# Performance work log

Hardware: AMD Instinct MI355X
Metric: run time of the kernel (lower is better)

Reference implementation:

```python
import jax, jax.numpy as jnp
import numpy as np

B, L = 4, 2048
D_MODEL, D_STATE, D_CONV, EXPAND = 1024, 16, 4, 2
D_INNER = EXPAND * D_MODEL
DT_RANK = D_MODEL // 16  # mamba-ssm default dt_rank = ceil(d_model/16)


def _mamba(x, in_w, conv_w, conv_b, xproj_w, dt_w, dt_b, A_log, D, out_w):
    # x: [B, L, d_model]; faithful port of mamba_ssm.Mamba forward (slow path math)
    di, ds = A_log.shape
    dt_rank = dt_w.shape[1]
    dc = conv_w.shape[1]
    xz = x @ in_w.T                          # [B, L, 2*di]
    xi, z = jnp.split(xz, 2, axis=-1)
    # causal depthwise conv over time
    xc = jnp.swapaxes(xi, 1, 2)              # [B, di, L]
    xc = jax.lax.conv_general_dilated(
        xc, conv_w[:, None, :], (1,), [(dc - 1, 0)],
        feature_group_count=di, dimension_numbers=('NCH', 'OIH', 'NCH'))
    xc = xc + conv_b[None, :, None]
    xi = jax.nn.silu(jnp.swapaxes(xc, 1, 2))  # [B, L, di]
    proj = xi @ xproj_w.T                    # [B, L, dt_rank + 2*ds]
    dt, Bm, Cm = jnp.split(proj, [dt_rank, dt_rank + ds], axis=-1)
    delta = jax.nn.softplus(dt @ dt_w.T + dt_b)  # [B, L, di]
    A = -jnp.exp(A_log)                      # [di, ds]

    def step(h, t):
        d_t, B_t, C_t, x_t = t               # [B,di],[B,ds],[B,ds],[B,di]
        h = jnp.exp(d_t[:, :, None] * A) * h + (d_t * x_t)[:, :, None] * B_t[:, None, :]
        return h, jnp.einsum('bds,bs->bd', h, C_t)

    xs = (jnp.swapaxes(delta, 0, 1), jnp.swapaxes(Bm, 0, 1),
          jnp.swapaxes(Cm, 0, 1), jnp.swapaxes(xi, 0, 1))
    h0 = jnp.zeros((x.shape[0], di, ds), x.dtype)
    _, ys = jax.lax.scan(step, h0, xs)       # ys: [L, B, di]
    y = jnp.swapaxes(ys, 0, 1) + xi * D
    y = y * jax.nn.silu(z)
    return y @ out_w.T


def setup_inputs() -> dict:
    ks = jax.random.split(jax.random.key(0), 24)

    def p(i, shape, scale=0.02):
        return jax.random.normal(ks[i], shape, jnp.float32) * scale

    inp = {
        'x': jax.random.normal(ks[0], (B, L, D_MODEL), jnp.float32),
        'ln_g': jnp.ones((D_MODEL,), jnp.float32),
        'ln_b': jnp.zeros((D_MODEL,), jnp.float32),
        'merge_w': p(1, (D_MODEL, 2 * D_MODEL)),
        'merge_b': jnp.zeros((D_MODEL,), jnp.float32),
    }
    for j, pre in enumerate(('fwd', 'bwd')):
        o = 2 + j * 8
        inp[pre + '_in_w'] = p(o, (2 * D_INNER, D_MODEL))
        inp[pre + '_conv_w'] = p(o + 1, (D_INNER, D_CONV), 0.3)
        inp[pre + '_conv_b'] = jnp.zeros((D_INNER,), jnp.float32)
        inp[pre + '_xproj_w'] = p(o + 2, (DT_RANK + 2 * D_STATE, D_INNER))
        inp[pre + '_dt_w'] = p(o + 3, (D_INNER, DT_RANK), 0.1)
        inp[pre + '_dt_b'] = -4.0 + p(o + 4, (D_INNER,), 0.5)
        inp[pre + '_A_log'] = jnp.broadcast_to(
            jnp.log(jnp.arange(1, D_STATE + 1, dtype=jnp.float32)), (D_INNER, D_STATE)) + 0.0
        inp[pre + '_D'] = jnp.ones((D_INNER,), jnp.float32)
        inp[pre + '_out_w'] = p(o + 5, (D_MODEL, D_INNER))
    return inp


def reference(x, ln_g, ln_b, merge_w, merge_b,
              fwd_in_w, fwd_conv_w, fwd_conv_b, fwd_xproj_w, fwd_dt_w, fwd_dt_b,
              fwd_A_log, fwd_D, fwd_out_w,
              bwd_in_w, bwd_conv_w, bwd_conv_b, bwd_xproj_w, bwd_dt_w, bwd_dt_b,
              bwd_A_log, bwd_D, bwd_out_w):
    mu = jnp.mean(x, axis=-1, keepdims=True)
    var = jnp.mean(jnp.square(x - mu), axis=-1, keepdims=True)
    xn = (x - mu) / jnp.sqrt(var + 1e-5) * ln_g + ln_b
    y_f = _mamba(xn, fwd_in_w, fwd_conv_w, fwd_conv_b, fwd_xproj_w, fwd_dt_w,
                 fwd_dt_b, fwd_A_log, fwd_D, fwd_out_w)
    y_b = jnp.flip(_mamba(jnp.flip(xn, 1), bwd_in_w, bwd_conv_w, bwd_conv_b,
                          bwd_xproj_w, bwd_dt_w, bwd_dt_b, bwd_A_log, bwd_D,
                          bwd_out_w), 1)
    y = jnp.concatenate([y_f, y_b], axis=-1) @ merge_w.T + merge_b
    return x + y
```

## Files before the change

kernel.cpp:

```cpp
#include <hip/hip_runtime.h>

typedef unsigned short u16;
typedef unsigned int u32;
typedef __attribute__((ext_vector_type(8))) short short8;
typedef __attribute__((ext_vector_type(8))) u16 ushort8v;
typedef __attribute__((ext_vector_type(4))) float float4v;
typedef __attribute__((ext_vector_type(4))) u16 ushort4v;

#define SEQ_L 2048
#define NTOK 8192
#define DMODEL 1024
#define DINNER 2048
#define NCH 32
#define CHL 64

__device__ __forceinline__ float bf2f(u16 v) { return __uint_as_float(((u32)v) << 16); }
__device__ __forceinline__ u16 f2bf(float f) {
    u32 u = __float_as_uint(f);
    return (u16)((u + 0x7FFFu + ((u >> 16) & 1u)) >> 16);
}
__device__ __forceinline__ float loadf(const void* p, size_t i, bool bf) {
    return bf ? bf2f(((const u16*)p)[i]) : ((const float*)p)[i];
}
__device__ __forceinline__ void gl2lds(const void* g, void* l) {
    __builtin_amdgcn_global_load_lds(
        (const __attribute__((address_space(1))) void*)g,
        (__attribute__((address_space(3))) void*)l, 16, 0, 0);
}

__global__ void detect_kernel(const u32* __restrict__ lng, int* __restrict__ flag) {
    if (threadIdx.x == 0) flag[0] = (lng[0] == 0x3F800000u) ? 0 : 1;
}

__global__ void cvt_kernel(const void* __restrict__ in, u16* __restrict__ out,
                           int n4, const int* __restrict__ flag) {
    int i = blockIdx.x * 256 + threadIdx.x;
    if (i >= n4) return;
    bool bf = flag[0] != 0;
    ushort4v o;
    if (bf) {
        o = ((const ushort4v*)in)[i];
    } else {
        float4v v = ((const float4v*)in)[i];
        o.x = f2bf(v.x); o.y = f2bf(v.y); o.z = f2bf(v.z); o.w = f2bf(v.w);
    }
    ((ushort4v*)out)[i] = o;
}

__global__ __launch_bounds__(256) void ln_kernel(const void* __restrict__ xin,
        const void* __restrict__ g, const void* __restrict__ be,
        u16* __restrict__ xn, const int* __restrict__ flag) {
    bool bf = flag[0] != 0;
    int tok = blockIdx.x;
    int tid = threadIdx.x;
    float v[4];
    if (bf) {
        ushort4v u = ((const ushort4v*)xin)[(size_t)tok * 256 + tid];
        v[0] = bf2f(u.x); v[1] = bf2f(u.y); v[2] = bf2f(u.z); v[3] = bf2f(u.w);
    } else {
        float4v f = ((const float4v*)xin)[(size_t)tok * 256 + tid];
        v[0] = f.x; v[1] = f.y; v[2] = f.z; v[3] = f.w;
    }
    float s = v[0] + v[1] + v[2] + v[3];
    float s2 = v[0]*v[0] + v[1]*v[1] + v[2]*v[2] + v[3]*v[3];
    for (int o = 1; o < 64; o <<= 1) { s += __shfl_xor(s, o); s2 += __shfl_xor(s2, o); }
    __shared__ float red[8];
    int w = tid >> 6;
    if ((tid & 63) == 0) { red[w] = s; red[4 + w] = s2; }
    __syncthreads();
    s = red[0] + red[1] + red[2] + red[3];
    s2 = red[4] + red[5] + red[6] + red[7];
    float mu = s * (1.f / 1024.f);
    float var = s2 * (1.f / 1024.f) - mu * mu;
    float rstd = rsqrtf(var + 1e-5f);
    int base = tid * 4;
    ushort4v o;
    o.x = f2bf((v[0] - mu) * rstd * loadf(g, base + 0, bf) + loadf(be, base + 0, bf));
    o.y = f2bf((v[1] - mu) * rstd * loadf(g, base + 1, bf) + loadf(be, base + 1, bf));
    o.z = f2bf((v[2] - mu) * rstd * loadf(g, base + 2, bf) + loadf(be, base + 2, bf));
    o.w = f2bf((v[3] - mu) * rstd * loadf(g, base + 3, bf) + loadf(be, base + 3, bf));
    ((ushort4v*)xn)[(size_t)tok * 256 + tid] = o;
}

__global__ __launch_bounds__(256) void build_wf(
    const void* __restrict__ dtw, const void* __restrict__ xpw,
    u16* __restrict__ wf, const int* __restrict__ flag)
{
    bool bf = flag[0] != 0;
    int n = blockIdx.x;
    int k0 = threadIdx.x * 8;
    ushort8v o;
    if (n >= DINNER) {
        int r = (n - DINNER) + 64;
        if (bf) {
            o = *(const ushort8v*)((const u16*)xpw + (size_t)r * 2048 + k0);
        } else {
            const float* p = (const float*)xpw + (size_t)r * 2048 + k0;
            #pragma unroll
            for (int j = 0; j < 8; ++j) o[j] = f2bf(p[j]);
        }
    } else {
        float acc[8];
        #pragma unroll
        for (int j = 0; j < 8; ++j) acc[j] = 0.f;
        for (int r = 0; r < 64; ++r) {
            float dw = loadf(dtw, (size_t)n * 64 + r, bf);
            if (bf) {
                ushort8v v = *(const ushort8v*)((const u16*)xpw + (size_t)r * 2048 + k0);
                #pragma unroll
                for (int j = 0; j < 8; ++j) acc[j] = fmaf(dw, bf2f(v[j]), acc[j]);
            } else {
                const float* p = (const float*)xpw + (size_t)r * 2048 + k0;
                #pragma unroll
                for (int j = 0; j < 8; ++j) acc[j] = fmaf(dw, p[j], acc[j]);
            }
        }
        #pragma unroll
        for (int j = 0; j < 8; ++j) o[j] = f2bf(acc[j]);
    }
    *(ushort8v*)(wf + (size_t)n * 2048 + k0) = o;
}

template<int EPI, bool FLIPA, bool FLIPC>
__global__ __launch_bounds__(256) void gemm_bt(
    const u16* __restrict__ A, int lda,
    const u16* __restrict__ W, int ldw,
    void* __restrict__ Cv, int ldc,
    int M, int N, int K,
    const void* __restrict__ bias, const void* __restrict__ resid,
    const int* __restrict__ flag)
{
    __shared__ u16 As[128 * 32];
    __shared__ u16 Ws[128 * 32];
    bool bf = flag[0] != 0;
    int tid = threadIdx.x;
    int lane = tid & 63;
    int wave = tid >> 6;
    int wm = wave >> 1, wn = wave & 1;
    int m0 = blockIdx.x * 128;
    int n0 = blockIdx.y * 128;
    int l15 = lane & 15;
    int quad = lane >> 4;

    int c0 = tid, c1 = tid + 256;
    int row0 = c0 >> 2, row1 = c1 >> 2;
    int kk0 = ((c0 & 3) ^ ((row0 ^ (row0 >> 1)) & 3)) << 3;
    int kk1 = ((c1 & 3) ^ ((row1 ^ (row1 >> 1)) & 3)) << 3;
    int ar0 = m0 + row0, ar1 = m0 + row1;
    if (FLIPA) {
        int b0 = ar0 >> 11, t0 = ar0 & (SEQ_L - 1); ar0 = (b0 << 11) | (SEQ_L - 1 - t0);
        int b1 = ar1 >> 11, t1 = ar1 & (SEQ_L - 1); ar1 = (b1 << 11) | (SEQ_L - 1 - t1);
    }
    int wr0 = n0 + row0; if (wr0 > N - 1) wr0 = N - 1;
    int wr1 = n0 + row1; if (wr1 > N - 1) wr1 = N - 1;
    const u16* Ag0 = A + (size_t)ar0 * lda + kk0;
    const u16* Ag1 = A + (size_t)ar1 * lda + kk1;
    const u16* Wg0 = W + (size_t)wr0 * ldw + kk0;
    const u16* Wg1 = W + (size_t)wr1 * ldw + kk1;
    u16* lA0 = &As[c0 * 8]; u16* lA1 = &As[c1 * 8];
    u16* lW0 = &Ws[c0 * 8]; u16* lW1 = &Ws[c1 * 8];

    int aoff[4], boff[4];
    #pragma unroll
    for (int i = 0; i < 4; ++i) {
        int ra = wm * 64 + i * 16 + l15;
        aoff[i] = ra * 32 + ((quad ^ ((ra ^ (ra >> 1)) & 3)) << 3);
        int rb = wn * 64 + i * 16 + l15;
        boff[i] = rb * 32 + ((quad ^ ((rb ^ (rb >> 1)) & 3)) << 3);
    }

    float4v acc[4][4] = {};

    for (int k0 = 0; k0 < K; k0 += 32) {
        __syncthreads();
        gl2lds(Ag0 + k0, lA0);
        gl2lds(Ag1 + k0, lA1);
        gl2lds(Wg0 + k0, lW0);
        gl2lds(Wg1 + k0, lW1);
        __syncthreads();
        short8 af[4], bfr[4];
        #pragma unroll
        for (int i = 0; i < 4; ++i) af[i] = *(const short8*)&As[aoff[i]];
        #pragma unroll
        for (int j = 0; j < 4; ++j) bfr[j] = *(const short8*)&Ws[boff[j]];
        #pragma unroll
        for (int i = 0; i < 4; ++i)
            #pragma unroll
            for (int j = 0; j < 4; ++j)
                acc[i][j] = __builtin_amdgcn_mfma_f32_16x16x32_bf16(af[i], bfr[j], acc[i][j], 0, 0, 0);
    }

    #pragma unroll
    for (int i = 0; i < 4; ++i) {
        #pragma unroll
        for (int j = 0; j < 4; ++j) {
            #pragma unroll
            for (int r = 0; r < 4; ++r) {
                int row = m0 + wm * 64 + i * 16 + quad * 4 + r;
                int col = n0 + wn * 64 + j * 16 + l15;
                if (col < N) {
                    float v = acc[i][j][r];
                    int orow = row;
                    if (FLIPC) { int bb = row >> 11; int t = row & (SEQ_L - 1); orow = (bb << 11) | (SEQ_L - 1 - t); }
                    if (EPI == 0) {
                        ((u16*)Cv)[(size_t)orow * ldc + col] = f2bf(v);
                    } else if (EPI == 2) {
                        v += loadf(bias, col, bf) + loadf(resid, (size_t)row * DMODEL + col, bf);
                        if (bf) ((u16*)Cv)[(size_t)orow * ldc + col] = f2bf(v);
                        else    ((float*)Cv)[(size_t)orow * ldc + col] = v;
                    } else {
                        if (col < DINNER) {
                            v += loadf(bias, col, bf);
                            v = (v > 20.f) ? v : log1pf(__expf(v));
                            ((u16*)Cv)[(size_t)orow * 4096 + col] = f2bf(v);
                        } else {
                            ((u16*)resid)[(size_t)orow * 32 + (col - DINNER)] = f2bf(v);
                        }
                    }
                }
            }
        }
    }
}

__global__ __launch_bounds__(256) void conv_kernel(const u16* __restrict__ xz,
        const void* __restrict__ cw, const void* __restrict__ cb,
        u16* __restrict__ xc, const int* __restrict__ flag)
{
    bool bf = flag[0] != 0;
    int idx = blockIdx.x * 256 + threadIdx.x;
    int d = idx & (DINNER - 1);
    int t = (idx >> 11) & (SEQ_L - 1);
    int b = idx >> 22;
    float acc = loadf(cb, d, bf);
    #pragma unroll
    for (int k = 0; k < 4; ++k) {
        int tt = t - 3 + k;
        if (tt >= 0)
            acc += loadf(cw, d * 4 + k, bf) * bf2f(xz[((size_t)(b * SEQ_L + tt) << 12) + d]);
    }
    float r = acc / (1.f + __expf(-acc));
    xc[idx] = f2bf(r);
}


__global__ __launch_bounds__(256) void scan_pass1(
    const u16* __restrict__ xz, const u16* __restrict__ xc,
    const u16* __restrict__ proj, const void* __restrict__ A_log,
    float2* __restrict__ chk, const int* __restrict__ flag)
{
    bool bf = flag[0] != 0;
    int g = blockIdx.x * 256 + threadIdx.x;
    int d = g & (DINNER - 1);
    int c = (g >> 11) & (NCH - 1);
    int b = g >> 16;
    float Ac[16];
    #pragma unroll
    for (int s = 0; s < 16; ++s) Ac[s] = -expf(loadf(A_log, (size_t)d * 16 + s, bf));
    size_t tok0 = (size_t)b * SEQ_L + c * CHL;
    const u16* dp = xz + tok0 * 4096 + d;
    const u16* xp = xc + tok0 * DINNER + d;
    const u16* bp = proj + tok0 * 32;
    float h[16];
    #pragma unroll
    for (int s = 0; s < 16; ++s) h[s] = 0.f;
    float sd = 0.f;
    for (int t = 0; t < CHL; ++t) {
        float dl = bf2f(*dp);
        float xi = bf2f(*xp);
        ushort8v bv0 = *(const ushort8v*)bp;
        ushort8v bv1 = *(const ushort8v*)(bp + 8);
        float u = dl * xi;
        #pragma unroll
        for (int s = 0; s < 16; ++s) {
            float a = __expf(dl * Ac[s]);
            float Bs = bf2f(s < 8 ? bv0[s] : bv1[s - 8]);
            h[s] = fmaf(a, h[s], u * Bs);
        }
        sd += dl;
        dp += 4096; xp += DINNER; bp += 32;
    }
    size_t base = (size_t)c * 131072 + ((size_t)b << 15) + d;
    #pragma unroll
    for (int s = 0; s < 16; ++s)
        chk[base + (size_t)s * 2048] = make_float2(__expf(Ac[s] * sd), h[s]);
}

__global__ __launch_bounds__(256) void scan_mid(float2* __restrict__ chk) {
    int g = blockIdx.x * 256 + threadIdx.x;
    float hi = 0.f;
    #pragma unroll 4
    for (int c = 0; c < NCH; ++c) {
        float2 v = chk[(size_t)c * 131072 + g];
        chk[(size_t)c * 131072 + g].x = hi;
        hi = fmaf(v.x, hi, v.y);
    }
}

__global__ __launch_bounds__(256) void scan_pass2(
    u16* __restrict__ xz, const u16* __restrict__ xc,
    const u16* __restrict__ proj, const void* __restrict__ A_log,
    const void* __restrict__ Dp, const float2* __restrict__ chk,
    const int* __restrict__ flag)
{
    bool bf = flag[0] != 0;
    int g = blockIdx.x * 256 + threadIdx.x;
    int d = g & (DINNER - 1);
    int c = (g >> 11) & (NCH - 1);
    int b = g >> 16;
    float Ac[16];
    #pragma unroll
    for (int s = 0; s < 16; ++s) Ac[s] = -expf(loadf(A_log, (size_t)d * 16 + s, bf));
    float Dd = loadf(Dp, d, bf);
    size_t tok0 = (size_t)b * SEQ_L + c * CHL;
    const u16* dp = xz + tok0 * 4096 + d;
    const u16* xp = xc + tok0 * DINNER + d;
    const u16* bp = proj + tok0 * 32;
    u16* zp = xz + tok0 * 4096 + DINNER + d;
    size_t base = (size_t)c * 131072 + ((size_t)b << 15) + d;
    float h[16];
    #pragma unroll
    for (int s = 0; s < 16; ++s) h[s] = chk[base + (size_t)s * 2048].x;
    for (int t = 0; t < CHL; ++t) {
        float dl = bf2f(*dp);
        float xi = bf2f(*xp);
        ushort8v bv0 = *(const ushort8v*)bp;
        ushort8v bv1 = *(const ushort8v*)(bp + 8);
        ushort8v cv0 = *(const ushort8v*)(bp + 16);
        ushort8v cv1 = *(const ushort8v*)(bp + 24);
        float u = dl * xi;
        float y0 = 0.f, y1 = 0.f;
        #pragma unroll
        for (int s = 0; s < 16; ++s) {
            float a = __expf(dl * Ac[s]);
            float Bs = bf2f(s < 8 ? bv0[s] : bv1[s - 8]);
            float Cs = bf2f(s < 8 ? cv0[s] : cv1[s - 8]);
            h[s] = fmaf(a, h[s], u * Bs);
            if (s & 1) y1 = fmaf(h[s], Cs, y1); else y0 = fmaf(h[s], Cs, y0);
        }
        float y = y0 + y1 + xi * Dd;
        float z = bf2f(*zp);
        *zp = f2bf(y * (z / (1.f + __expf(-z))));
        dp += 4096; xp += DINNER; bp += 32; zp += 4096;
    }
}

extern "C" void kernel_launch(void* const* d_in, const int* in_sizes, int n_in,
                              void* d_out, int out_size, void* d_ws, size_t ws_size,
                              hipStream_t stream) {
    (void)in_sizes; (void)n_in; (void)out_size;
    const void* x = d_in[0];
    const void* ln_g = d_in[1];
    const void* ln_be = d_in[2];
    const void* merge_w = d_in[3];
    const void* merge_b = d_in[4];
    const void* in_w[2]   = {d_in[5],  d_in[14]};
    const void* conv_w[2] = {d_in[6],  d_in[15]};
    const void* conv_b[2] = {d_in[7],  d_in[16]};
    const void* xproj_w[2]= {d_in[8],  d_in[17]};
    const void* dt_w[2]   = {d_in[9],  d_in[18]};
    const void* dt_bias[2]= {d_in[10], d_in[19]};
    const void* A_log[2]  = {d_in[11], d_in[20]};
    const void* Dp[2]     = {d_in[12], d_in[21]};
    const void* out_w[2]  = {d_in[13], d_in[22]};

    char* wsb = (char*)d_ws;
    size_t off = 0;
    auto alloc = [&](size_t bytes) -> void* {
        void* p = wsb + off; off += (bytes + 255) & ~(size_t)255; return p;
    };
    int* flag     = (int*)alloc(256);
    u16* xzb      = (u16*)alloc((size_t)NTOK * 4096 * 2);
    u16* xcb      = (u16*)alloc((size_t)NTOK * 2048 * 2);
    u16* projb    = (u16*)alloc((size_t)NTOK * 32 * 2);
    float2* chk   = (float2*)alloc((size_t)NCH * 131072 * 8);
    u16* ycat     = (u16*)alloc((size_t)NTOK * 2048 * 2);
    u16* wf       = (u16*)alloc((size_t)2080 * 2048 * 2);
    if (off > ws_size) return;
    u16* xn = (u16*)d_out;

    u16* w_in  = (u16*)((char*)chk);
    u16* w_out = (u16*)((char*)chk + (8u << 20));
    u16* w_mg  = (u16*)((char*)chk + (12u << 20));

    detect_kernel<<<1, 64, 0, stream>>>((const u32*)ln_g, flag);
    ln_kernel<<<dim3(NTOK), 256, 0, stream>>>(x, ln_g, ln_be, xn, flag);

    auto cvt = [&](const void* src, u16* dst, int n) {
        cvt_kernel<<<dim3(n / 1024), 256, 0, stream>>>(src, dst, n / 4, flag);
    };

    for (int dd = 0; dd < 2; ++dd) {
        cvt(in_w[dd], w_in, 4096 * 1024);
        if (dd == 0)
            gemm_bt<0,false,false><<<dim3(64,32), 256, 0, stream>>>(xn, 1024, w_in, 1024, xzb, 4096, NTOK, 4096, 1024, nullptr, nullptr, flag);
        else
            gemm_bt<0,true,false><<<dim3(64,32), 256, 0, stream>>>(xn, 1024, w_in, 1024, xzb, 4096, NTOK, 4096, 1024, nullptr, nullptr, flag);
        conv_kernel<<<dim3((NTOK * DINNER) / 256), 256, 0, stream>>>(xzb, conv_w[dd], conv_b[dd], xcb, flag);
        build_wf<<<dim3(2080), 256, 0, stream>>>(dt_w[dd], xproj_w[dd], wf, flag);
        gemm_bt<3,false,false><<<dim3(64,17), 256, 0, stream>>>(xcb, 2048, wf, 2048, xzb, 4096, NTOK, 2080, 2048, dt_bias[dd], projb, flag);
        scan_pass1<<<dim3(1024), 256, 0, stream>>>(xzb, xcb, projb, A_log[dd], chk, flag);
        scan_mid<<<dim3(512), 256, 0, stream>>>(chk);
        scan_pass2<<<dim3(1024), 256, 0, stream>>>(xzb, xcb, projb, A_log[dd], Dp[dd], chk, flag);
        cvt(out_w[dd], w_out, 1024 * 2048);
        if (dd == 0)
            gemm_bt<0,false,false><<<dim3(64,8), 256, 0, stream>>>(xzb + DINNER, 4096, w_out, 2048, ycat, 2048, NTOK, 1024, 2048, nullptr, nullptr, flag);
        else
            gemm_bt<0,false,true><<<dim3(64,8), 256, 0, stream>>>(xzb + DINNER, 4096, w_out, 2048, ycat + 1024, 2048, NTOK, 1024, 2048, nullptr, nullptr, flag);
    }
    cvt(merge_w, w_mg, 1024 * 2048);
    gemm_bt<2,false,false><<<dim3(64,8), 256, 0, stream>>>(ycat, 2048, w_mg, 2048, d_out, 1024, NTOK, 1024, 2048, merge_b, x, flag);
}
```

Baseline: 1.442 ms.

## Fold merge projection into out_proj weights and accumulate directly into output

```diff
diff --git a/kernel.cpp b/kernel.cpp
--- a/kernel.cpp
+++ b/kernel.cpp
@@ -45,6 +45,27 @@
         o.x = f2bf(v.x); o.y = f2bf(v.y); o.z = f2bf(v.z); o.w = f2bf(v.w);
     }
     ((ushort4v*)out)[i] = o;
+}
+
+__global__ __launch_bounds__(256) void transpose_ow(const void* __restrict__ ow,
+        u16* __restrict__ ot, const int* __restrict__ flag) {
+    bool bf = flag[0] != 0;
+    __shared__ u16 tile[32][33];
+    int k0 = blockIdx.x * 32;
+    int j0 = blockIdx.y * 32;
+    int tx = threadIdx.x & 31;
+    int ty = threadIdx.x >> 5;
+    #pragma unroll
+    for (int r = 0; r < 4; ++r) {
+        int j = ty + r * 8;
+        tile[j][tx] = f2bf(loadf(ow, (size_t)(j0 + j) * 2048 + k0 + tx, bf));
+    }
+    __syncthreads();
+    #pragma unroll
+    for (int r = 0; r < 4; ++r) {
+        int k = ty + r * 8;
+        ot[(size_t)(k0 + k) * 1024 + j0 + tx] = tile[tx][k];
+    }
 }
 
 __global__ __launch_bounds__(256) void ln_kernel(const void* __restrict__ xin,
@@ -121,7 +142,7 @@
     *(ushort8v*)(wf + (size_t)n * 2048 + k0) = o;
 }
 
-template<int EPI, bool FLIPA, bool FLIPC>
+template<int EPI, bool FLIPA>
 __global__ __launch_bounds__(256) void gemm_bt(
     const u16* __restrict__ A, int lda,
     const u16* __restrict__ W, int ldw,
@@ -200,21 +221,27 @@
                 int col = n0 + wn * 64 + j * 16 + l15;
                 if (col < N) {
                     float v = acc[i][j][r];
-                    int orow = row;
-                    if (FLIPC) { int bb = row >> 11; int t = row & (SEQ_L - 1); orow = (bb << 11) | (SEQ_L - 1 - t); }
                     if (EPI == 0) {
-                        ((u16*)Cv)[(size_t)orow * ldc + col] = f2bf(v);
+                        ((u16*)Cv)[(size_t)row * ldc + col] = f2bf(v);
                     } else if (EPI == 2) {
                         v += loadf(bias, col, bf) + loadf(resid, (size_t)row * DMODEL + col, bf);
-                        if (bf) ((u16*)Cv)[(size_t)orow * ldc + col] = f2bf(v);
-                        else    ((float*)Cv)[(size_t)orow * ldc + col] = v;
-                    } else {
+                        if (bf) ((u16*)Cv)[(size_t)row * ldc + col] = f2bf(v);
+                        else    ((float*)Cv)[(size_t)row * ldc + col] = v;
+                    } else if (EPI == 3) {
                         if (col < DINNER) {
                             v += loadf(bias, col, bf);
-                            v = (v > 20.f) ? v : log1pf(__expf(v));
-                            ((u16*)Cv)[(size_t)orow * 4096 + col] = f2bf(v);
+                            v = fmaxf(v, 0.f) + __logf(1.f + __expf(-fabsf(v)));
+                            ((u16*)Cv)[(size_t)row * 4096 + col] = f2bf(v);
                         } else {
-                            ((u16*)resid)[(size_t)orow * 32 + (col - DINNER)] = f2bf(v);
+                            ((u16*)resid)[(size_t)row * 32 + (col - DINNER)] = f2bf(v);
+                        }
+                    } else {
+                        if (bf) {
+                            u16* p = (u16*)Cv + (size_t)row * ldc + col;
+                            *p = f2bf(bf2f(*p) + v);
+                        } else {
+                            float* p = (float*)Cv + (size_t)row * ldc + col;
+                            *p = *p + v;
                         }
                     }
                 }
@@ -256,7 +283,7 @@
     int b = g >> 16;
     float Ac[16];
     #pragma unroll
-    for (int s = 0; s < 16; ++s) Ac[s] = -expf(loadf(A_log, (size_t)d * 16 + s, bf));
+    for (int s = 0; s < 16; ++s) Ac[s] = -__expf(loadf(A_log, (size_t)d * 16 + s, bf));
     size_t tok0 = (size_t)b * SEQ_L + c * CHL;
     const u16* dp = xz + tok0 * 4096 + d;
     const u16* xp = xc + tok0 * DINNER + d;
@@ -310,7 +337,7 @@
     int b = g >> 16;
     float Ac[16];
     #pragma unroll
-    for (int s = 0; s < 16; ++s) Ac[s] = -expf(loadf(A_log, (size_t)d * 16 + s, bf));
+    for (int s = 0; s < 16; ++s) Ac[s] = -__expf(loadf(A_log, (size_t)d * 16 + s, bf));
     float Dd = loadf(Dp, d, bf);
     size_t tok0 = (size_t)b * SEQ_L + c * CHL;
     const u16* dp = xz + tok0 * 4096 + d;
@@ -374,14 +401,15 @@
     u16* xcb      = (u16*)alloc((size_t)NTOK * 2048 * 2);
     u16* projb    = (u16*)alloc((size_t)NTOK * 32 * 2);
     float2* chk   = (float2*)alloc((size_t)NCH * 131072 * 8);
-    u16* ycat     = (u16*)alloc((size_t)NTOK * 2048 * 2);
     u16* wf       = (u16*)alloc((size_t)2080 * 2048 * 2);
+    u16* wof[2]   = {(u16*)alloc((size_t)1024 * 2048 * 2),
+                     (u16*)alloc((size_t)1024 * 2048 * 2)};
+    u16* xn       = (u16*)alloc((size_t)NTOK * DMODEL * 2);
+    u16* w_mgc    = (u16*)alloc((size_t)1024 * 2048 * 2);
+    u16* outT     = (u16*)alloc((size_t)2048 * 1024 * 2);
     if (off > ws_size) return;
-    u16* xn = (u16*)d_out;
-
-    u16* w_in  = (u16*)((char*)chk);
-    u16* w_out = (u16*)((char*)chk + (8u << 20));
-    u16* w_mg  = (u16*)((char*)chk + (12u << 20));
+
+    u16* w_in = (u16*)chk;
 
     detect_kernel<<<1, 64, 0, stream>>>((const u32*)ln_g, flag);
     ln_kernel<<<dim3(NTOK), 256, 0, stream>>>(x, ln_g, ln_be, xn, flag);
@@ -390,24 +418,29 @@
         cvt_kernel<<<dim3(n / 1024), 256, 0, stream>>>(src, dst, n / 4, flag);
     };
 
+    cvt(merge_w, w_mgc, 1024 * 2048);
+    for (int dd = 0; dd < 2; ++dd) {
+        transpose_ow<<<dim3(64, 32), 256, 0, stream>>>(out_w[dd], outT, flag);
+        gemm_bt<0,false><<<dim3(8, 16), 256, 0, stream>>>(
+            w_mgc + dd * 1024, 2048, outT, 1024, wof[dd], 2048, 1024, 2048, 1024,
+            nullptr, nullptr, flag);
+    }
+
     for (int dd = 0; dd < 2; ++dd) {
         cvt(in_w[dd], w_in, 4096 * 1024);
         if (dd == 0)
-            gemm_bt<0,false,false><<<dim3(64,32), 256, 0, stream>>>(xn, 1024, w_in, 1024, xzb, 4096, NTOK, 4096, 1024, nullptr, nullptr, flag);
+            gemm_bt<0,false><<<dim3(64,32), 256, 0, stream>>>(xn, 1024, w_in, 1024, xzb, 4096, NTOK, 4096, 1024, nullptr, nullptr, flag);
         else
-            gemm_bt<0,true,false><<<dim3(64,32), 256, 0, stream>>>(xn, 1024, w_in, 1024, xzb, 4096, NTOK, 4096, 1024, nullptr, nullptr, flag);
+            gemm_bt<0,true><<<dim3(64,32), 256, 0, stream>>>(xn, 1024, w_in, 1024, xzb, 4096, NTOK, 4096, 1024, nullptr, nullptr, flag);
         conv_kernel<<<dim3((NTOK * DINNER) / 256), 256, 0, stream>>>(xzb, conv_w[dd], conv_b[dd], xcb, flag);
         build_wf<<<dim3(2080), 256, 0, stream>>>(dt_w[dd], xproj_w[dd], wf, flag);
-        gemm_bt<3,false,false><<<dim3(64,17), 256, 0, stream>>>(xcb, 2048, wf, 2048, xzb, 4096, NTOK, 2080, 2048, dt_bias[dd], projb, flag);
+        gemm_bt<3,false><<<dim3(64,17), 256, 0, stream>>>(xcb, 2048, wf, 2048, xzb, 4096, NTOK, 2080, 2048, dt_bias[dd], projb, flag);
         scan_pass1<<<dim3(1024), 256, 0, stream>>>(xzb, xcb, projb, A_log[dd], chk, flag);
         scan_mid<<<dim3(512), 256, 0, stream>>>(chk);
         scan_pass2<<<dim3(1024), 256, 0, stream>>>(xzb, xcb, projb, A_log[dd], Dp[dd], chk, flag);
-        cvt(out_w[dd], w_out, 1024 * 2048);
         if (dd == 0)
-            gemm_bt<0,false,false><<<dim3(64,8), 256, 0, stream>>>(xzb + DINNER, 4096, w_out, 2048, ycat, 2048, NTOK, 1024, 2048, nullptr, nullptr, flag);
+            gemm_bt<2,false><<<dim3(64,8), 256, 0, stream>>>(xzb + DINNER, 4096, wof[0], 2048, d_out, 1024, NTOK, 1024, 2048, merge_b, x, flag);
         else
-            gemm_bt<0,false,true><<<dim3(64,8), 256, 0, stream>>>(xzb + DINNER, 4096, w_out, 2048, ycat + 1024, 2048, NTOK, 1024, 2048, nullptr, nullptr, flag);
-    }
-    cvt(merge_w, w_mg, 1024 * 2048);
-    gemm_bt<2,false,false><<<dim3(64,8), 256, 0, stream>>>(ycat, 2048, w_mg, 2048, d_out, 1024, NTOK, 1024, 2048, merge_b, x, flag);
-}
+            gemm_bt<5,true><<<dim3(64,8), 256, 0, stream>>>(xzb + DINNER, 4096, wof[1], 2048, d_out, 1024, NTOK, 1024, 2048, nullptr, nullptr, flag);
+    }
+}
```

Result: faster. 1.394 ms (-3.3%).
